# Optimization experiments

Hardware: AMD Instinct MI355X
Metric: run time of the kernel (lower is better)

The kernel has to match this reference:

```python
import jax, jax.numpy as jnp
import numpy as np

B, DX, DY, H, T, L = 256, 256, 256, 512, 128, 2
EPS = 1e-5


def setup_inputs() -> dict:
    key = jax.random.key(0)
    ks = jax.random.split(key, 16)
    s = 0.02
    return {
        "inputx": jax.random.normal(ks[0], (B, DX, T), dtype=jnp.float32),
        "inputy": jax.random.normal(ks[1], (B, DY, T), dtype=jnp.float32),
        # stacked gate weights: f,i,o for T-path and F-path, [L, 3H, Dx+Dy+H]
        "WTg": jax.random.normal(ks[2], (L, 3 * H, DX + DY + H), dtype=jnp.float32) * s,
        "bTg": jax.random.normal(ks[3], (L, 3 * H), dtype=jnp.float32) * s,
        "WFg": jax.random.normal(ks[4], (L, 3 * H, DX + DY + H), dtype=jnp.float32) * s,
        "bFg": jax.random.normal(ks[5], (L, 3 * H), dtype=jnp.float32) * s,
        # candidate cell weights
        "WTc": jax.random.normal(ks[6], (L, H, DX + H), dtype=jnp.float32) * s,
        "bTc": jax.random.normal(ks[7], (L, H), dtype=jnp.float32) * s,
        "WFc": jax.random.normal(ks[8], (L, H, DY + H), dtype=jnp.float32) * s,
        "bFc": jax.random.normal(ks[9], (L, H), dtype=jnp.float32) * s,
        # batchnorm affine params per layer
        "gammaT": jnp.ones((L, H), dtype=jnp.float32),
        "betaT": jnp.zeros((L, H), dtype=jnp.float32),
        "gammaF": jnp.ones((L, H), dtype=jnp.float32),
        "betaF": jnp.zeros((L, H), dtype=jnp.float32),
    }


def _batchnorm(h, gamma, beta):
    # train-mode BN over batch dim, biased variance (torch semantics)
    mu = jnp.mean(h, axis=0, keepdims=True)
    var = jnp.mean((h - mu) ** 2, axis=0, keepdims=True)
    return (h - mu) * jax.lax.rsqrt(var + EPS) * gamma + beta


def _forward(inputx, inputy, WTg, bTg, WFg, bFg, WTc, bTc, WFc, bFc,
             gammaT, betaT, gammaF, betaF):
    nL = WTg.shape[0]
    b, h = inputx.shape[0], gammaT.shape[1]
    zeros = jnp.zeros((nL, b, h), dtype=inputx.dtype)

    def step(carry, xy):
        hT, hF, CT, CF = carry  # each [L, B, H]
        x, y = xy  # [B, Dx], [B, Dy]
        hT_n, hF_n, CT_n, CF_n = [], [], [], []
        for i in range(nL):
            catT = jnp.concatenate([x, y, hT[i]], axis=1)
            catF = jnp.concatenate([x, y, hF[i]], axis=1)
            gT = jax.nn.sigmoid(catT @ WTg[i].T + bTg[i])  # [B, 3H]
            gF = jax.nn.sigmoid(catF @ WFg[i].T + bFg[i])
            fT, iT, oT = jnp.split(gT, 3, axis=1)
            fF, iF, oF = jnp.split(gF, 3, axis=1)
            cT = jnp.tanh(jnp.concatenate([x, hT[i]], axis=1) @ WTc[i].T + bTc[i])
            cF = jnp.tanh(jnp.concatenate([y, hF[i]], axis=1) @ WFc[i].T + bFc[i])
            CTi = fT * CT[i] + iT * cT
            CFi = fF * CF[i] + iF * cF
            hTi = oT * jnp.tanh(CTi)
            hFi = oF * jnp.tanh(CFi)
            hT_n.append(hTi); hF_n.append(hFi); CT_n.append(CTi); CF_n.append(CFi)
        hT = jnp.stack(hT_n); hF = jnp.stack(hF_n)
        CT = jnp.stack(CT_n); CF = jnp.stack(CF_n)
        # output comes from last layer only; BN in train mode
        outT = _batchnorm(hT[-1], gammaT[-1], betaT[-1])
        outF = _batchnorm(hF[-1], gammaF[-1], betaF[-1])
        return (hT, hF, CT, CF), (outT, outF)

    xs = (jnp.transpose(inputx, (2, 0, 1)), jnp.transpose(inputy, (2, 0, 1)))
    _, (outT_seq, outF_seq) = jax.lax.scan(step, (zeros, zeros, zeros, zeros), xs)
    # [T, B, H] -> [B, H, T] (torch.stack(..., dim=2))
    return jnp.transpose(outT_seq, (1, 2, 0)), jnp.transpose(outF_seq, (1, 2, 0))


def reference(inputx, inputy, WTg, bTg, WFg, bFg, WTc, bTc, WFc, bFc,
              gammaT, betaT, gammaF, betaF):
    return _forward(inputx, inputy, WTg, bTg, WFg, bFg, WTc, bTc, WFc, bFc,
                    gammaT, betaT, gammaF, betaF)
```

## Files before the change

kernel.cpp:

```cpp
#include <hip/hip_runtime.h>

#define NBLK 256
#define NTHR 512

typedef __attribute__((ext_vector_type(8))) short s16x8;
typedef __attribute__((ext_vector_type(8))) __bf16 bf16x8;
typedef __attribute__((ext_vector_type(4))) float f32x4;

__device__ __forceinline__ ushort f2bf(float f) {
  uint u = __float_as_uint(f);
  return (ushort)((u + 0x7FFFu + ((u >> 16) & 1u)) >> 16);
}
__device__ __forceinline__ float bf2f(ushort s) {
  return __uint_as_float(((uint)s) << 16);
}
__device__ __forceinline__ float sigm(float x) { return 1.f / (1.f + __expf(-x)); }
__device__ __forceinline__ float tanhf_(float x) {
  x = fminf(9.f, fmaxf(-9.f, x));
  float e = __expf(2.f * x);
  return (e - 1.f) / (e + 1.f);
}

__global__ void init_k(uint* __restrict__ bar) {
  int i = blockIdx.x * blockDim.x + threadIdx.x;
  if (i < 512) bar[i] = 0u;
}

__global__ void xyt_k(const float* __restrict__ x, const float* __restrict__ y,
                      ushort* __restrict__ xyT) {
  __shared__ ushort sT[64 * 130];
  const int bid = blockIdx.x;
  const int chunk = bid & 7;
  const int b = bid >> 3;
  const int d0 = (chunk & 3) * 64;
  const float* src = ((chunk < 4) ? x : y) + ((size_t)b * 256 + d0) * 128;
  const int tid = threadIdx.x;
  const int tt = tid & 127, rr = tid >> 7;
#pragma unroll
  for (int i = 0; i < 32; ++i) {
    int row = i * 2 + rr;
    sT[row * 130 + tt] = f2bf(src[(size_t)row * 128 + tt]);
  }
  __syncthreads();
  const int dbase = ((chunk < 4) ? 0 : 256) + d0;
#pragma unroll
  for (int i = 0; i < 16; ++i) {
    int idx = tid + i * 256;
    int t = idx >> 5, j = idx & 31;
    uint v = (uint)sT[(2 * j) * 130 + t] | ((uint)sT[(2 * j + 1) * 130 + t] << 16);
    *(uint*)(xyT + ((size_t)t * 256 + b) * 512 + dbase + 2 * j) = v;
  }
}

__launch_bounds__(NTHR, 2)
__global__ void seq_k(const ushort* __restrict__ xyT, ushort* __restrict__ hbuf,
                      ushort* __restrict__ hist,
                      const float* __restrict__ WTg, const float* __restrict__ WFg,
                      const float* __restrict__ WTc, const float* __restrict__ WFc,
                      const float* __restrict__ bTg, const float* __restrict__ bFg,
                      const float* __restrict__ bTc, const float* __restrict__ bFc,
                      uint* bar) {
  extern __shared__ char smem[];
  float* sAcc = (float*)(smem + 98304);

  const int tid = threadIdx.x;
  const int bid = blockIdx.x;
  const int mt = bid & 7;
  const int cg = (bid >> 3) & 15;
  const int s = bid >> 7;
  const int g = s * 8 + mt;
  const int m0 = mt * 32;
  const int j0 = cg * 32;
  const int w = tid >> 6;
  const int l = tid & 63;
  const int l15 = l & 15;
  const int q16 = (l >> 4) * 16;
  const bool isGate = (w < 6);
  uint* fl = bar + (g << 4);

  s16x8 wreg[32];
  if (isGate) {
    const int gt = w >> 1, half = w & 1;
    const float* Wp = ((s == 0) ? WTg : WFg) + 1572864
                    + ((size_t)(gt * 512 + j0 + half * 16 + l15)) * 1024 + (q16 >> 1);
#pragma unroll
    for (int kk = 0; kk < 32; ++kk) {
      s16x8 v;
#pragma unroll
      for (int e = 0; e < 8; ++e) v[e] = (short)f2bf(Wp[kk * 32 + e]);
      wreg[kk] = v;
    }
  } else {
    const int half = w & 1;
    const float* Wp = ((s == 0) ? WTc : WFc) + 393216
                    + ((size_t)(j0 + half * 16 + l15)) * 768 + (q16 >> 1);
#pragma unroll
    for (int kk = 0; kk < 24; ++kk) {
      s16x8 v;
#pragma unroll
      for (int e = 0; e < 8; ++e) v[e] = (short)f2bf(Wp[kk * 32 + e]);
      wreg[kk] = v;
    }
  }

  const int ro = tid >> 4;
  const int cc0 = (tid & 15) * 2;
  const int ehalf = cc0 >> 4;
  const int ec16 = cc0 & 15;
  float bfv0, bfv1, biv0, biv1, bov0, bov1, bcv0, bcv1;
  {
    const float* bg = ((s == 0) ? bTg : bFg) + 1536;
    const float* bc = ((s == 0) ? bTc : bFc) + 512;
    int col = j0 + cc0;
    bfv0 = bg[col];        bfv1 = bg[col + 1];
    biv0 = bg[512 + col];  biv1 = bg[513 + col];
    bov0 = bg[1024 + col]; bov1 = bg[1025 + col];
    bcv0 = bc[col];        bcv1 = bc[col + 1];
  }
  float C0 = 0.f, C1 = 0.f;

  auto stage_row = [&](const ushort* gbase, char* lbase, int r) {
    const char* srow = (const char*)(gbase + (size_t)r * 512);
    int off = (l * 16) ^ ((r & 7) << 4);
    __builtin_amdgcn_global_load_lds(
        (const __attribute__((address_space(1))) void*)(srow + off),
        (__attribute__((address_space(3))) void*)(lbase + (r << 10)), 16, 0, 0);
  };
  auto stage_row_coh = [&](const ushort* gbase, char* lbase, int r) {
    const char* srow = (const char*)(gbase + (size_t)r * 512);
    int off = (l * 16) ^ ((r & 7) << 4);
    __builtin_amdgcn_global_load_lds(
        (const __attribute__((address_space(1))) void*)(srow + off),
        (__attribute__((address_space(3))) void*)(lbase + (r << 10)), 16, 0, 17);
  };

  {
#pragma unroll
    for (int i = 0; i < 4; ++i) stage_row(xyT + (size_t)m0 * 512, smem, (w << 2) + i);
  }
  __syncthreads();

  const int sw = (l15 & 7) << 4;
  for (int t = 0; t < 128; ++t) {
    const int cur = t & 1;
    char* xyb = smem + cur * 32768;
    char* xybn = smem + (cur ^ 1) * 32768;
    char* hb = smem + 65536;

    f32x4 acc0 = {0.f, 0.f, 0.f, 0.f};
    f32x4 acc1 = {0.f, 0.f, 0.f, 0.f};

    {
      const char* base0 = xyb + (l15 << 10);
      const char* base1 = xyb + ((16 + l15) << 10);
      if (isGate) {
#pragma unroll
        for (int kk = 0; kk < 16; ++kk) {
          int c2 = (kk * 64 + q16) ^ sw;
          s16x8 a0 = *(const s16x8*)(base0 + c2);
          s16x8 a1 = *(const s16x8*)(base1 + c2);
          acc0 = __builtin_amdgcn_mfma_f32_16x16x32_bf16(
              __builtin_bit_cast(bf16x8, a0), __builtin_bit_cast(bf16x8, wreg[kk]), acc0, 0, 0, 0);
          acc1 = __builtin_amdgcn_mfma_f32_16x16x32_bf16(
              __builtin_bit_cast(bf16x8, a1), __builtin_bit_cast(bf16x8, wreg[kk]), acc1, 0, 0, 0);
        }
      } else {
#pragma unroll
        for (int kk = 0; kk < 8; ++kk) {
          int c2 = ((s * 512 + kk * 64 + q16)) ^ sw;
          s16x8 a0 = *(const s16x8*)(base0 + c2);
          s16x8 a1 = *(const s16x8*)(base1 + c2);
          acc0 = __builtin_amdgcn_mfma_f32_16x16x32_bf16(
              __builtin_bit_cast(bf16x8, a0), __builtin_bit_cast(bf16x8, wreg[kk]), acc0, 0, 0, 0);
          acc1 = __builtin_amdgcn_mfma_f32_16x16x32_bf16(
              __builtin_bit_cast(bf16x8, a1), __builtin_bit_cast(bf16x8, wreg[kk]), acc1, 0, 0, 0);
        }
      }
    }

    const int tn = (t < 127) ? t + 1 : 127;
    const ushort* xyNext = xyT + ((size_t)(tn * 256 + m0)) * 512;
    if (w != 0) {
#pragma unroll
      for (int i = 0; i < 4; ++i) stage_row(xyNext, xybn, (w << 2) + i);
    }

    if (w == 0 && t) {
      const uint tgt = (uint)t;
      while (true) {
        uint v = (l < 16)
                     ? __hip_atomic_load(fl + l, __ATOMIC_RELAXED, __HIP_MEMORY_SCOPE_SYSTEM)
                     : tgt;
        if (__all((int)(v >= tgt))) break;
        __builtin_amdgcn_s_sleep(1);
      }
    }
    __syncthreads();

    if (w == 0) {
#pragma unroll
      for (int i = 0; i < 4; ++i) stage_row(xyNext, xybn, i);
    }
    if (t) {
      const ushort* hsrc = hbuf + ((size_t)((cur * 2 + s) * 256 + m0)) * 512;
#pragma unroll
      for (int i = 0; i < 4; ++i) stage_row_coh(hsrc, hb, (w << 2) + i);
    }

    __syncthreads();

    if (t) {
      const char* base0 = hb + (l15 << 10);
      const char* base1 = hb + ((16 + l15) << 10);
      if (isGate) {
#pragma unroll
        for (int kk = 0; kk < 16; ++kk) {
          int c2 = (kk * 64 + q16) ^ sw;
          s16x8 a0 = *(const s16x8*)(base0 + c2);
          s16x8 a1 = *(const s16x8*)(base1 + c2);
          acc0 = __builtin_amdgcn_mfma_f32_16x16x32_bf16(
              __builtin_bit_cast(bf16x8, a0), __builtin_bit_cast(bf16x8, wreg[16 + kk]), acc0, 0, 0, 0);
          acc1 = __builtin_amdgcn_mfma_f32_16x16x32_bf16(
              __builtin_bit_cast(bf16x8, a1), __builtin_bit_cast(bf16x8, wreg[16 + kk]), acc1, 0, 0, 0);
        }
      } else {
#pragma unroll
        for (int kk = 0; kk < 16; ++kk) {
          int c2 = (kk * 64 + q16) ^ sw;
          s16x8 a0 = *(const s16x8*)(base0 + c2);
          s16x8 a1 = *(const s16x8*)(base1 + c2);
          acc0 = __builtin_amdgcn_mfma_f32_16x16x32_bf16(
              __builtin_bit_cast(bf16x8, a0), __builtin_bit_cast(bf16x8, wreg[8 + kk]), acc0, 0, 0, 0);
          acc1 = __builtin_amdgcn_mfma_f32_16x16x32_bf16(
              __builtin_bit_cast(bf16x8, a1), __builtin_bit_cast(bf16x8, wreg[8 + kk]), acc1, 0, 0, 0);
        }
      }
    }

#pragma unroll
    for (int rg = 0; rg < 4; ++rg) {
      sAcc[w * 576 + ((q16 >> 2) + rg) * 18 + l15] = acc0[rg];
      sAcc[w * 576 + (16 + (q16 >> 2) + rg) * 18 + l15] = acc1[rg];
    }
    __syncthreads();

    {
      const float2 pf = *(const float2*)&sAcc[(0 + ehalf) * 576 + ro * 18 + ec16];
      const float2 pi = *(const float2*)&sAcc[(2 + ehalf) * 576 + ro * 18 + ec16];
      const float2 po = *(const float2*)&sAcc[(4 + ehalf) * 576 + ro * 18 + ec16];
      const float2 pc = *(const float2*)&sAcc[(6 + ehalf) * 576 + ro * 18 + ec16];
      float f0 = sigm(pf.x + bfv0), f1 = sigm(pf.y + bfv1);
      float i0 = sigm(pi.x + biv0), i1 = sigm(pi.y + biv1);
      float o0 = sigm(po.x + bov0), o1 = sigm(po.y + bov1);
      float c0 = tanhf_(pc.x + bcv0), c1 = tanhf_(pc.y + bcv1);
      C0 = f0 * C0 + i0 * c0;
      C1 = f1 * C1 + i1 * c1;
      float h0 = o0 * tanhf_(C0);
      float h1 = o1 * tanhf_(C1);
      uint hp = (uint)f2bf(h0) | (((uint)f2bf(h1)) << 16);
      __hip_atomic_store(
          (uint*)(hbuf + ((size_t)(((cur ^ 1) * 2 + s) * 256 + m0 + ro)) * 512 + j0 + cc0), hp,
          __ATOMIC_RELAXED, __HIP_MEMORY_SCOPE_SYSTEM);
      __builtin_nontemporal_store(
          hp, (uint*)(hist + (((size_t)s * 128 + t) * 256 + m0 + ro) * 512 + j0 + cc0));
    }
    __syncthreads();
    if (tid == 0)
      __hip_atomic_store(fl + cg, (uint)(t + 1), __ATOMIC_RELAXED, __HIP_MEMORY_SCOPE_SYSTEM);
  }
}

__global__ void bnstat_k(const ushort* __restrict__ hist,
                         const float* __restrict__ gT, const float* __restrict__ beT,
                         const float* __restrict__ gF, const float* __restrict__ beF,
                         float* __restrict__ scale, float* __restrict__ shift) {
  const int t = blockIdx.x >> 1, s = blockIdx.x & 1;
  const int tid = threadIdx.x;
  const ushort* hp = hist + ((size_t)s * 128 + t) * 256 * 512;
  const float* gp = (s ? gF : gT) + 512;
  const float* bp = (s ? beF : beT) + 512;
#pragma unroll
  for (int hh = 0; hh < 2; ++hh) {
    const int h = tid + hh * 256;
    float sum = 0.f, sq = 0.f;
#pragma unroll 8
    for (int b = 0; b < 256; ++b) {
      float v = bf2f(hp[(size_t)b * 512 + h]);
      sum += v;
      sq += v * v;
    }
    float mu = sum * 0.00390625f;
    float var = sq * 0.00390625f - mu * mu;
    float sc = (1.0f / sqrtf(var + 1e-5f)) * gp[h];
    size_t o = ((size_t)s * 128 + t) * 512 + h;
    scale[o] = sc;
    shift[o] = bp[h] - mu * sc;
  }
}

__global__ void bnwrite_k(const ushort* __restrict__ hist, const float* __restrict__ scale,
                          const float* __restrict__ shift, float* __restrict__ out) {
  __shared__ float sT[64 * 129];
  const int bid = blockIdx.x;
  const int hc = bid & 7, b = (bid >> 3) & 255, s = bid >> 11;
  const int h0 = hc * 64;
  const int tid = threadIdx.x;
  const int hh = tid & 63, tq = tid >> 6;
#pragma unroll 4
  for (int tc = 0; tc < 32; ++tc) {
    const int t = tc * 4 + tq;
    const size_t so = ((size_t)s * 128 + t) * 512 + h0 + hh;
    float v = bf2f(hist[(((size_t)s * 128 + t) * 256 + b) * 512 + h0 + hh]);
    sT[hh * 129 + t] = v * scale[so] + shift[so];
  }
  __syncthreads();
  const int t2 = tid & 127, hq = tid >> 7;
#pragma unroll 4
  for (int i = 0; i < 32; ++i) {
    const int h = i * 2 + hq;
    out[(size_t)s * 16777216 + ((size_t)b * 512 + h0 + h) * 128 + t2] = sT[h * 129 + t2];
  }
}

extern "C" void kernel_launch(void* const* d_in, const int* in_sizes, int n_in,
                              void* d_out, int out_size, void* d_ws, size_t ws_size,
                              hipStream_t stream) {
  const float* inputx = (const float*)d_in[0];
  const float* inputy = (const float*)d_in[1];
  const float* WTg = (const float*)d_in[2];
  const float* bTg = (const float*)d_in[3];
  const float* WFg = (const float*)d_in[4];
  const float* bFg = (const float*)d_in[5];
  const float* WTc = (const float*)d_in[6];
  const float* bTc = (const float*)d_in[7];
  const float* WFc = (const float*)d_in[8];
  const float* bFc = (const float*)d_in[9];
  const float* gT = (const float*)d_in[10];
  const float* beT = (const float*)d_in[11];
  const float* gF = (const float*)d_in[12];
  const float* beF = (const float*)d_in[13];
  float* out = (float*)d_out;

  char* ws = (char*)d_ws;
  ushort* xyT = (ushort*)ws;
  ushort* hbuf = (ushort*)(ws + 33554432);
  ushort* hist = (ushort*)(ws + 34603008);
  float* scale = (float*)(ws + 101711872);
  float* shift = (float*)(ws + 102236160);
  uint* bar = (uint*)(ws + 102760448);

  init_k<<<2, 256, 0, stream>>>(bar);
  xyt_k<<<2048, 256, 0, stream>>>(inputx, inputy, xyT);

  hipFuncSetAttribute((const void*)seq_k, hipFuncAttributeMaxDynamicSharedMemorySize, 116736);
  void* args[12];
  args[0] = &xyT; args[1] = &hbuf; args[2] = &hist;
  args[3] = &WTg; args[4] = &WFg; args[5] = &WTc; args[6] = &WFc;
  args[7] = &bTg; args[8] = &bFg; args[9] = &bTc; args[10] = &bFc;
  args[11] = &bar;
  hipLaunchCooperativeKernel((const void*)seq_k, dim3(NBLK), dim3(NTHR), args, 116736, stream);

  bnstat_k<<<256, 256, 0, stream>>>(hist, gT, beT, gF, beF, scale, shift);
  bnwrite_k<<<4096, 256, 0, stream>>>(hist, scale, shift, out);
}
```

Before: 648.0 us.

## Use agent-scope coherence for h exchange when a group shares one XCD

At startup each block records its XCC id into a per-group bitmask and waits for all 16 group members, then decides whether the whole group lives on a single XCD. If it does, the recurrent h exchange, flag polling and stores use agent scope and a cheaper cache policy instead of system scope. This is meant to cut the coherence cost of the per-step cross-block handoff. The change also reorders the h staging ahead of the x staging and drops the nontemporal hint on history stores. If the workgroups are spread across XCDs, the fast path never triggers and only the startup barrier is added.

Measured after the change: 855.1 us. +32.0%, slower.

```diff
diff --git a/kernel.cpp b/kernel.cpp
--- a/kernel.cpp
+++ b/kernel.cpp
@@ -6,6 +6,8 @@
 typedef __attribute__((ext_vector_type(8))) short s16x8;
 typedef __attribute__((ext_vector_type(8))) __bf16 bf16x8;
 typedef __attribute__((ext_vector_type(4))) float f32x4;
+
+template <bool B> struct BoolC { static constexpr bool value = B; };
 
 __device__ __forceinline__ ushort f2bf(float f) {
   uint u = __float_as_uint(f);
@@ -62,6 +64,7 @@
                       uint* bar) {
   extern __shared__ char smem[];
   float* sAcc = (float*)(smem + 98304);
+  uint* sCoh = (uint*)(smem + 116736);
 
   const int tid = threadIdx.x;
   const int bid = blockIdx.x;
@@ -78,6 +81,19 @@
   const bool isGate = (w < 6);
   uint* fl = bar + (g << 4);
 
+  {
+    uint xcc = __builtin_amdgcn_s_getreg((3u << 11) | 20u) & 15u;
+    uint* gw = bar + 256 + (g << 3);
+    if (tid == 0) {
+      __hip_atomic_fetch_or(gw, 1u << xcc, __ATOMIC_RELAXED, __HIP_MEMORY_SCOPE_SYSTEM);
+      __hip_atomic_fetch_add(gw + 1, 1u, __ATOMIC_RELEASE, __HIP_MEMORY_SCOPE_SYSTEM);
+      while (__hip_atomic_load(gw + 1, __ATOMIC_RELAXED, __HIP_MEMORY_SCOPE_SYSTEM) < 16u)
+        __builtin_amdgcn_s_sleep(8);
+      uint mask = __hip_atomic_load(gw, __ATOMIC_RELAXED, __HIP_MEMORY_SCOPE_SYSTEM);
+      sCoh[0] = (uint)(__popc(mask) == 1);
+    }
+  }
+
   s16x8 wreg[32];
   if (isGate) {
     const int gt = w >> 1, half = w & 1;
@@ -126,148 +142,160 @@
         (const __attribute__((address_space(1))) void*)(srow + off),
         (__attribute__((address_space(3))) void*)(lbase + (r << 10)), 16, 0, 0);
   };
-  auto stage_row_coh = [&](const ushort* gbase, char* lbase, int r) {
-    const char* srow = (const char*)(gbase + (size_t)r * 512);
-    int off = (l * 16) ^ ((r & 7) << 4);
-    __builtin_amdgcn_global_load_lds(
-        (const __attribute__((address_space(1))) void*)(srow + off),
-        (__attribute__((address_space(3))) void*)(lbase + (r << 10)), 16, 0, 17);
+
+  {
+#pragma unroll
+    for (int i = 0; i < 4; ++i) stage_row(xyT + (size_t)m0 * 512, smem, (w << 2) + i);
+  }
+  __syncthreads();
+  const bool fastCoh = (sCoh[0] != 0);
+
+  const int sw = (l15 & 7) << 4;
+
+  auto run = [&](auto FASTC) {
+    constexpr bool F = decltype(FASTC)::value;
+    constexpr int SCOPE = F ? __HIP_MEMORY_SCOPE_AGENT : __HIP_MEMORY_SCOPE_SYSTEM;
+
+    auto stage_row_h = [&](const ushort* gbase, char* lbase, int r) {
+      const char* srow = (const char*)(gbase + (size_t)r * 512);
+      int off = (l * 16) ^ ((r & 7) << 4);
+      if constexpr (F)
+        __builtin_amdgcn_global_load_lds(
+            (const __attribute__((address_space(1))) void*)(srow + off),
+            (__attribute__((address_space(3))) void*)(lbase + (r << 10)), 16, 0, 1);
+      else
+        __builtin_amdgcn_global_load_lds(
+            (const __attribute__((address_space(1))) void*)(srow + off),
+            (__attribute__((address_space(3))) void*)(lbase + (r << 10)), 16, 0, 17);
+    };
+
+    for (int t = 0; t < 128; ++t) {
+      const int cur = t & 1;
+      char* xyb = smem + cur * 32768;
+      char* xybn = smem + (cur ^ 1) * 32768;
+      char* hb = smem + 65536;
+
+      f32x4 acc0 = {0.f, 0.f, 0.f, 0.f};
+      f32x4 acc1 = {0.f, 0.f, 0.f, 0.f};
+
+      {
+        const char* base0 = xyb + (l15 << 10);
+        const char* base1 = xyb + ((16 + l15) << 10);
+        if (isGate) {
+#pragma unroll
+          for (int kk = 0; kk < 16; ++kk) {
+            int c2 = (kk * 64 + q16) ^ sw;
+            s16x8 a0 = *(const s16x8*)(base0 + c2);
+            s16x8 a1 = *(const s16x8*)(base1 + c2);
+            acc0 = __builtin_amdgcn_mfma_f32_16x16x32_bf16(
+                __builtin_bit_cast(bf16x8, a0), __builtin_bit_cast(bf16x8, wreg[kk]), acc0, 0, 0, 0);
+            acc1 = __builtin_amdgcn_mfma_f32_16x16x32_bf16(
+                __builtin_bit_cast(bf16x8, a1), __builtin_bit_cast(bf16x8, wreg[kk]), acc1, 0, 0, 0);
+          }
+        } else {
+#pragma unroll
+          for (int kk = 0; kk < 8; ++kk) {
+            int c2 = ((s * 512 + kk * 64 + q16)) ^ sw;
+            s16x8 a0 = *(const s16x8*)(base0 + c2);
+            s16x8 a1 = *(const s16x8*)(base1 + c2);
+            acc0 = __builtin_amdgcn_mfma_f32_16x16x32_bf16(
+                __builtin_bit_cast(bf16x8, a0), __builtin_bit_cast(bf16x8, wreg[kk]), acc0, 0, 0, 0);
+            acc1 = __builtin_amdgcn_mfma_f32_16x16x32_bf16(
+                __builtin_bit_cast(bf16x8, a1), __builtin_bit_cast(bf16x8, wreg[kk]), acc1, 0, 0, 0);
+          }
+        }
+      }
+
+      const int tn = (t < 127) ? t + 1 : 127;
+      const ushort* xyNext = xyT + ((size_t)(tn * 256 + m0)) * 512;
+      if (w != 0) {
+#pragma unroll
+        for (int i = 0; i < 4; ++i) stage_row(xyNext, xybn, (w << 2) + i);
+      }
+
+      if (w == 0 && t) {
+        const uint tgt = (uint)t;
+        while (true) {
+          uint v = (l < 16) ? __hip_atomic_load(fl + l, __ATOMIC_RELAXED, SCOPE) : tgt;
+          if (__all((int)(v >= tgt))) break;
+          __builtin_amdgcn_s_sleep(1);
+        }
+      }
+      __syncthreads();
+
+      if (t) {
+        const ushort* hsrc = hbuf + ((size_t)((cur * 2 + s) * 256 + m0)) * 512;
+#pragma unroll
+        for (int i = 0; i < 4; ++i) stage_row_h(hsrc, hb, (w << 2) + i);
+      }
+      if (w == 0) {
+#pragma unroll
+        for (int i = 0; i < 4; ++i) stage_row(xyNext, xybn, i);
+      }
+
+      __syncthreads();
+
+      if (t) {
+        const char* base0 = hb + (l15 << 10);
+        const char* base1 = hb + ((16 + l15) << 10);
+        if (isGate) {
+#pragma unroll
+          for (int kk = 0; kk < 16; ++kk) {
+            int c2 = (kk * 64 + q16) ^ sw;
+            s16x8 a0 = *(const s16x8*)(base0 + c2);
+            s16x8 a1 = *(const s16x8*)(base1 + c2);
+            acc0 = __builtin_amdgcn_mfma_f32_16x16x32_bf16(
+                __builtin_bit_cast(bf16x8, a0), __builtin_bit_cast(bf16x8, wreg[16 + kk]), acc0, 0, 0, 0);
+            acc1 = __builtin_amdgcn_mfma_f32_16x16x32_bf16(
+                __builtin_bit_cast(bf16x8, a1), __builtin_bit_cast(bf16x8, wreg[16 + kk]), acc1, 0, 0, 0);
+          }
+        } else {
+#pragma unroll
+          for (int kk = 0; kk < 16; ++kk) {
+            int c2 = (kk * 64 + q16) ^ sw;
+            s16x8 a0 = *(const s16x8*)(base0 + c2);
+            s16x8 a1 = *(const s16x8*)(base1 + c2);
+            acc0 = __builtin_amdgcn_mfma_f32_16x16x32_bf16(
+                __builtin_bit_cast(bf16x8, a0), __builtin_bit_cast(bf16x8, wreg[8 + kk]), acc0, 0, 0, 0);
+            acc1 = __builtin_amdgcn_mfma_f32_16x16x32_bf16(
+                __builtin_bit_cast(bf16x8, a1), __builtin_bit_cast(bf16x8, wreg[8 + kk]), acc1, 0, 0, 0);
+          }
+        }
+      }
+
+#pragma unroll
+      for (int rg = 0; rg < 4; ++rg) {
+        sAcc[w * 576 + ((q16 >> 2) + rg) * 18 + l15] = acc0[rg];
+        sAcc[w * 576 + (16 + (q16 >> 2) + rg) * 18 + l15] = acc1[rg];
+      }
+      __syncthreads();
+
+      {
+        const float2 pf = *(const float2*)&sAcc[(0 + ehalf) * 576 + ro * 18 + ec16];
+        const float2 pi = *(const float2*)&sAcc[(2 + ehalf) * 576 + ro * 18 + ec16];
+        const float2 po = *(const float2*)&sAcc[(4 + ehalf) * 576 + ro * 18 + ec16];
+        const float2 pc = *(const float2*)&sAcc[(6 + ehalf) * 576 + ro * 18 + ec16];
+        float f0 = sigm(pf.x + bfv0), f1 = sigm(pf.y + bfv1);
+        float i0 = sigm(pi.x + biv0), i1 = sigm(pi.y + biv1);
+        float o0 = sigm(po.x + bov0), o1 = sigm(po.y + bov1);
+        float c0 = tanhf_(pc.x + bcv0), c1 = tanhf_(pc.y + bcv1);
+        C0 = f0 * C0 + i0 * c0;
+        C1 = f1 * C1 + i1 * c1;
+        float h0 = o0 * tanhf_(C0);
+        float h1 = o1 * tanhf_(C1);
+        uint hp = (uint)f2bf(h0) | (((uint)f2bf(h1)) << 16);
+        __hip_atomic_store(
+            (uint*)(hbuf + ((size_t)(((cur ^ 1) * 2 + s) * 256 + m0 + ro)) * 512 + j0 + cc0), hp,
+            __ATOMIC_RELAXED, SCOPE);
+        *(uint*)(hist + (((size_t)s * 128 + t) * 256 + m0 + ro) * 512 + j0 + cc0) = hp;
+      }
+      __syncthreads();
+      if (tid == 0) __hip_atomic_store(fl + cg, (uint)(t + 1), __ATOMIC_RELAXED, SCOPE);
+    }
   };
 
-  {
-#pragma unroll
-    for (int i = 0; i < 4; ++i) stage_row(xyT + (size_t)m0 * 512, smem, (w << 2) + i);
-  }
-  __syncthreads();
-
-  const int sw = (l15 & 7) << 4;
-  for (int t = 0; t < 128; ++t) {
-    const int cur = t & 1;
-    char* xyb = smem + cur * 32768;
-    char* xybn = smem + (cur ^ 1) * 32768;
-    char* hb = smem + 65536;
-
-    f32x4 acc0 = {0.f, 0.f, 0.f, 0.f};
-    f32x4 acc1 = {0.f, 0.f, 0.f, 0.f};
-
-    {
-      const char* base0 = xyb + (l15 << 10);
-      const char* base1 = xyb + ((16 + l15) << 10);
-      if (isGate) {
-#pragma unroll
-        for (int kk = 0; kk < 16; ++kk) {
-          int c2 = (kk * 64 + q16) ^ sw;
-          s16x8 a0 = *(const s16x8*)(base0 + c2);
-          s16x8 a1 = *(const s16x8*)(base1 + c2);
-          acc0 = __builtin_amdgcn_mfma_f32_16x16x32_bf16(
-              __builtin_bit_cast(bf16x8, a0), __builtin_bit_cast(bf16x8, wreg[kk]), acc0, 0, 0, 0);
-          acc1 = __builtin_amdgcn_mfma_f32_16x16x32_bf16(
-              __builtin_bit_cast(bf16x8, a1), __builtin_bit_cast(bf16x8, wreg[kk]), acc1, 0, 0, 0);
-        }
-      } else {
-#pragma unroll
-        for (int kk = 0; kk < 8; ++kk) {
-          int c2 = ((s * 512 + kk * 64 + q16)) ^ sw;
-          s16x8 a0 = *(const s16x8*)(base0 + c2);
-          s16x8 a1 = *(const s16x8*)(base1 + c2);
-          acc0 = __builtin_amdgcn_mfma_f32_16x16x32_bf16(
-              __builtin_bit_cast(bf16x8, a0), __builtin_bit_cast(bf16x8, wreg[kk]), acc0, 0, 0, 0);
-          acc1 = __builtin_amdgcn_mfma_f32_16x16x32_bf16(
-              __builtin_bit_cast(bf16x8, a1), __builtin_bit_cast(bf16x8, wreg[kk]), acc1, 0, 0, 0);
-        }
-      }
-    }
-
-    const int tn = (t < 127) ? t + 1 : 127;
-    const ushort* xyNext = xyT + ((size_t)(tn * 256 + m0)) * 512;
-    if (w != 0) {
-#pragma unroll
-      for (int i = 0; i < 4; ++i) stage_row(xyNext, xybn, (w << 2) + i);
-    }
-
-    if (w == 0 && t) {
-      const uint tgt = (uint)t;
-      while (true) {
-        uint v = (l < 16)
-                     ? __hip_atomic_load(fl + l, __ATOMIC_RELAXED, __HIP_MEMORY_SCOPE_SYSTEM)
-                     : tgt;
-        if (__all((int)(v >= tgt))) break;
-        __builtin_amdgcn_s_sleep(1);
-      }
-    }
-    __syncthreads();
-
-    if (w == 0) {
-#pragma unroll
-      for (int i = 0; i < 4; ++i) stage_row(xyNext, xybn, i);
-    }
-    if (t) {
-      const ushort* hsrc = hbuf + ((size_t)((cur * 2 + s) * 256 + m0)) * 512;
-#pragma unroll
-      for (int i = 0; i < 4; ++i) stage_row_coh(hsrc, hb, (w << 2) + i);
-    }
-
-    __syncthreads();
-
-    if (t) {
-      const char* base0 = hb + (l15 << 10);
-      const char* base1 = hb + ((16 + l15) << 10);
-      if (isGate) {
-#pragma unroll
-        for (int kk = 0; kk < 16; ++kk) {
-          int c2 = (kk * 64 + q16) ^ sw;
-          s16x8 a0 = *(const s16x8*)(base0 + c2);
-          s16x8 a1 = *(const s16x8*)(base1 + c2);
-          acc0 = __builtin_amdgcn_mfma_f32_16x16x32_bf16(
-              __builtin_bit_cast(bf16x8, a0), __builtin_bit_cast(bf16x8, wreg[16 + kk]), acc0, 0, 0, 0);
-          acc1 = __builtin_amdgcn_mfma_f32_16x16x32_bf16(
-              __builtin_bit_cast(bf16x8, a1), __builtin_bit_cast(bf16x8, wreg[16 + kk]), acc1, 0, 0, 0);
-        }
-      } else {
-#pragma unroll
-        for (int kk = 0; kk < 16; ++kk) {
-          int c2 = (kk * 64 + q16) ^ sw;
-          s16x8 a0 = *(const s16x8*)(base0 + c2);
-          s16x8 a1 = *(const s16x8*)(base1 + c2);
-          acc0 = __builtin_amdgcn_mfma_f32_16x16x32_bf16(
-              __builtin_bit_cast(bf16x8, a0), __builtin_bit_cast(bf16x8, wreg[8 + kk]), acc0, 0, 0, 0);
-          acc1 = __builtin_amdgcn_mfma_f32_16x16x32_bf16(
-              __builtin_bit_cast(bf16x8, a1), __builtin_bit_cast(bf16x8, wreg[8 + kk]), acc1, 0, 0, 0);
-        }
-      }
-    }
-
-#pragma unroll
-    for (int rg = 0; rg < 4; ++rg) {
-      sAcc[w * 576 + ((q16 >> 2) + rg) * 18 + l15] = acc0[rg];
-      sAcc[w * 576 + (16 + (q16 >> 2) + rg) * 18 + l15] = acc1[rg];
-    }
-    __syncthreads();
-
-    {
-      const float2 pf = *(const float2*)&sAcc[(0 + ehalf) * 576 + ro * 18 + ec16];
-      const float2 pi = *(const float2*)&sAcc[(2 + ehalf) * 576 + ro * 18 + ec16];
-      const float2 po = *(const float2*)&sAcc[(4 + ehalf) * 576 + ro * 18 + ec16];
-      const float2 pc = *(const float2*)&sAcc[(6 + ehalf) * 576 + ro * 18 + ec16];
-      float f0 = sigm(pf.x + bfv0), f1 = sigm(pf.y + bfv1);
-      float i0 = sigm(pi.x + biv0), i1 = sigm(pi.y + biv1);
-      float o0 = sigm(po.x + bov0), o1 = sigm(po.y + bov1);
-      float c0 = tanhf_(pc.x + bcv0), c1 = tanhf_(pc.y + bcv1);
-      C0 = f0 * C0 + i0 * c0;
-      C1 = f1 * C1 + i1 * c1;
-      float h0 = o0 * tanhf_(C0);
-      float h1 = o1 * tanhf_(C1);
-      uint hp = (uint)f2bf(h0) | (((uint)f2bf(h1)) << 16);
-      __hip_atomic_store(
-          (uint*)(hbuf + ((size_t)(((cur ^ 1) * 2 + s) * 256 + m0 + ro)) * 512 + j0 + cc0), hp,
-          __ATOMIC_RELAXED, __HIP_MEMORY_SCOPE_SYSTEM);
-      __builtin_nontemporal_store(
-          hp, (uint*)(hist + (((size_t)s * 128 + t) * 256 + m0 + ro) * 512 + j0 + cc0));
-    }
-    __syncthreads();
-    if (tid == 0)
-      __hip_atomic_store(fl + cg, (uint)(t + 1), __ATOMIC_RELAXED, __HIP_MEMORY_SCOPE_SYSTEM);
-  }
+  if (fastCoh) run(BoolC<true>{});
+  else run(BoolC<false>{});
 }
 
 __global__ void bnstat_k(const ushort* __restrict__ hist,
@@ -352,13 +380,13 @@
   init_k<<<2, 256, 0, stream>>>(bar);
   xyt_k<<<2048, 256, 0, stream>>>(inputx, inputy, xyT);
 
-  hipFuncSetAttribute((const void*)seq_k, hipFuncAttributeMaxDynamicSharedMemorySize, 116736);
+  hipFuncSetAttribute((const void*)seq_k, hipFuncAttributeMaxDynamicSharedMemorySize, 116800);
   void* args[12];
   args[0] = &xyT; args[1] = &hbuf; args[2] = &hist;
   args[3] = &WTg; args[4] = &WFg; args[5] = &WTc; args[6] = &WFc;
   args[7] = &bTg; args[8] = &bFg; args[9] = &bTc; args[10] = &bFc;
   args[11] = &bar;
-  hipLaunchCooperativeKernel((const void*)seq_k, dim3(NBLK), dim3(NTHR), args, 116736, stream);
+  hipLaunchCooperativeKernel((const void*)seq_k, dim3(NBLK), dim3(NTHR), args, 116800, stream);
 
   bnstat_k<<<256, 256, 0, stream>>>(hist, gT, beT, gF, beF, scale, shift);
   bnwrite_k<<<4096, 256, 0, stream>>>(hist, scale, shift, out);
```
